# Performance work log

Hardware: AMD Instinct MI355X
Metric: run time of the kernel (lower is better)

## Reference

```python
import jax, jax.numpy as jnp
import numpy as np

B_SZ, L, D_MODEL = 2, 2048, 1024
EXPAND, N_STATE, K = 2, 16, 4
D_INNER = D_MODEL * EXPAND


def setup_inputs() -> dict:
    key = jax.random.key(0)
    ks = jax.random.split(key, 12)
    s = lambda k, shape, scale=0.02: jax.random.normal(k, shape, jnp.float32) * scale
    return {
        "x": jax.random.normal(ks[0], (B_SZ, L, D_MODEL), jnp.float32),
        "ln_gamma": jnp.ones((D_MODEL,), jnp.float32),
        "ln_beta": jnp.zeros((D_MODEL,), jnp.float32),
        "W_in": s(ks[1], (D_MODEL, 2 * D_INNER)),
        "conv_w": s(ks[2], (D_INNER, 1, K), 0.1),
        "conv_b": jnp.zeros((D_INNER,), jnp.float32),
        "A_log": jax.random.normal(ks[3], (N_STATE,), jnp.float32),
        "B_mat": s(ks[4], (N_STATE, D_INNER), 0.05),
        "C_mat": s(ks[5], (D_INNER, N_STATE), 0.05),
        "D_vec": s(ks[6], (D_INNER,), 0.1),
        "Wd": s(ks[7], (D_INNER, D_INNER)),
        "bd": jnp.zeros((D_INNER,), jnp.float32),
        "W_out": s(ks[8], (D_INNER, D_MODEL)),
    }


def _layernorm(x, g, b, eps=1e-5):
    mu = jnp.mean(x, axis=-1, keepdims=True)
    var = jnp.var(x, axis=-1, keepdims=True)
    return (x - mu) * jax.lax.rsqrt(var + eps) * g + b


def _selective_scan(x, delta, A, B_mat, C_mat, D_vec):
    # x: (b,l,d), delta: (b,l), A: (n,)
    dA = jnp.exp(delta[..., None] * A)            # (b,l,n)
    Bx = jnp.einsum('bld,nd->bln', x, B_mat) * delta[..., None]  # (b,l,n)

    def step(h, inp):
        dA_t, Bx_t = inp
        h = dA_t * h + Bx_t
        return h, h

    h0 = jnp.zeros((x.shape[0], A.shape[0]), x.dtype)
    # scan over seq axis
    _, hs = jax.lax.scan(step, h0, (jnp.swapaxes(dA, 0, 1), jnp.swapaxes(Bx, 0, 1)))
    hs = jnp.swapaxes(hs, 0, 1)                   # (b,l,n)
    return jnp.einsum('bln,dn->bld', hs, C_mat) + D_vec * x


def reference(x, ln_gamma, ln_beta, W_in, conv_w, conv_b, A_log, B_mat, C_mat, D_vec, Wd, bd, W_out):
    residual = x
    h = _layernorm(x, ln_gamma, ln_beta)
    xg = h @ W_in                                  # (b,l,2*d_inner)
    xs, gate = jnp.split(xg, 2, axis=-1)
    # depthwise causal conv (torch pads K-1 both sides then slices [:L] == left pad K-1)
    xc = jnp.swapaxes(xs, 1, 2)                    # (b,d,l)
    xc = jax.lax.conv_general_dilated(
        xc, conv_w, window_strides=(1,), padding=((K - 1, 0),),
        dimension_numbers=('NCH', 'OIH', 'NCH'), feature_group_count=D_INNER)
    xc = xc + conv_b[None, :, None]
    xs = jnp.swapaxes(xc, 1, 2)                    # (b,l,d)
    xs = jax.nn.silu(xs)
    # S4 kernel
    delta = jnp.mean(jax.nn.softplus(xs @ Wd + bd), axis=-1)  # (b,l)
    A = -jnp.exp(A_log)
    y = _selective_scan(xs, delta, A, B_mat, C_mat, D_vec)
    y = y * jax.nn.silu(gate)
    y = y @ W_out
    return residual + y
```

## Files before the change

kernel.cpp:

```cpp
#include <hip/hip_runtime.h>
#include <cstdint>
#include <cstddef>

typedef unsigned short u16;
typedef __attribute__((ext_vector_type(4))) float floatx4;
typedef __attribute__((ext_vector_type(8))) __bf16 bf16x8;

__device__ __forceinline__ float u2f(u16 u) {
    union { unsigned int i; float f; } x;
    x.i = ((unsigned int)u) << 16;
    return x.f;
}
__device__ __forceinline__ u16 f2u(float f) {
    union { float f; unsigned int i; } x;
    x.f = f;
    unsigned int r = x.i + 0x7fffu + ((x.i >> 16) & 1u);
    return (u16)(r >> 16);
}

__device__ __forceinline__ void swz(int bid, int& x, int& y) {
    int xcd = bid & 7;
    int lid = bid >> 3;
    x = lid >> 2;
    y = xcd * 4 + (lid & 3);
}

__device__ __forceinline__ void tr_tile(const float* __restrict__ in, u16* __restrict__ out,
                                        int K, int N, int bx, int by, float* tile ) {
    int n0 = bx * 32, k0 = by * 32;
    int t = threadIdx.x;
    int r = t >> 3, c4 = (t & 7) * 4;
    float4 v = *(const float4*)(in + (size_t)(k0 + r) * N + n0 + c4);
    tile[r * 33 + c4 + 0] = v.x;
    tile[r * 33 + c4 + 1] = v.y;
    tile[r * 33 + c4 + 2] = v.z;
    tile[r * 33 + c4 + 3] = v.w;
    __syncthreads();
    int n = t >> 3, kg = (t & 7) * 4;
    ushort4 o;
    o.x = f2u(tile[(kg + 0) * 33 + n]);
    o.y = f2u(tile[(kg + 1) * 33 + n]);
    o.z = f2u(tile[(kg + 2) * 33 + n]);
    o.w = f2u(tile[(kg + 3) * 33 + n]);
    *(ushort4*)(out + (size_t)(n0 + n) * K + k0 + kg) = o;
}

__global__ __launch_bounds__(256)
void prep_kernel(const float* __restrict__ W_in, u16* __restrict__ Wt_in,
                 const float* __restrict__ Wd, u16* __restrict__ Wt_ext,
                 const float* __restrict__ W_out, u16* __restrict__ Wt_out,
                 const float* __restrict__ B_mat,
                 const float* __restrict__ x, const float* __restrict__ gamma,
                 const float* __restrict__ beta, u16* __restrict__ h,
                 float* __restrict__ out) {
    __shared__ float tile[32 * 33];
    int blk = blockIdx.x, t = threadIdx.x;
    if (blk < 4096) {
        tr_tile(W_in, Wt_in, 1024, 4096, blk & 127, blk >> 7, tile);
    } else if (blk < 8192) {
        int b2 = blk - 4096;
        tr_tile(Wd, Wt_ext, 2048, 2048, b2 & 63, b2 >> 6, tile);
    } else if (blk < 10240) {
        int b3 = blk - 8192;
        tr_tile(W_out, Wt_out, 2048, 1024, b3 & 31, b3 >> 5, tile);
    } else if (blk < 14336) {
        int r = blk - 10240;
        const float4* xr = (const float4*)(x + (size_t)r * 1024);
        float4 xv = xr[t];
        ((float4*)(out + (size_t)r * 1024))[t] = xv;
        float s = xv.x + xv.y + xv.z + xv.w;
        float ss = xv.x * xv.x + xv.y * xv.y + xv.z * xv.z + xv.w * xv.w;
#pragma unroll
        for (int off = 32; off > 0; off >>= 1) {
            s += __shfl_down(s, off, 64);
            ss += __shfl_down(ss, off, 64);
        }
        __shared__ float rs[4], rss[4], mu_s, ri_s;
        int wave = t >> 6, lane = t & 63;
        if (lane == 0) { rs[wave] = s; rss[wave] = ss; }
        __syncthreads();
        if (t == 0) {
            float S = rs[0] + rs[1] + rs[2] + rs[3];
            float SS = rss[0] + rss[1] + rss[2] + rss[3];
            float mu = S * (1.f / 1024.f);
            float var = SS * (1.f / 1024.f) - mu * mu;
            mu_s = mu;
            ri_s = rsqrtf(fmaxf(var, 0.f) + 1e-5f);
        }
        __syncthreads();
        float mu = mu_s, ri = ri_s;
        float4 gv = ((const float4*)gamma)[t];
        float4 bv = ((const float4*)beta)[t];
        ushort4 o;
        o.x = f2u((xv.x - mu) * ri * gv.x + bv.x);
        o.y = f2u((xv.y - mu) * ri * gv.y + bv.y);
        o.z = f2u((xv.z - mu) * ri * gv.z + bv.z);
        o.w = f2u((xv.w - mu) * ri * gv.w + bv.w);
        ((ushort4*)(h + (size_t)r * 1024))[t] = o;
    } else {
        int idx = (blk - 14336) * 256 + t;
        int row = 2048 + (idx >> 11), col = idx & 2047;
        u16 v = (row < 2064) ? f2u(B_mat[(size_t)(row - 2048) * 2048 + col]) : (u16)0;
        Wt_ext[(size_t)row * 2048 + col] = v;
    }
}

__device__ __forceinline__ void gl_lds16(const u16* g, u16* l) {
    __builtin_amdgcn_global_load_lds(
        (const __attribute__((address_space(1))) void*)g,
        (__attribute__((address_space(3))) void*)l, 16, 0, 0);
}

template <int EPI>
__device__ __forceinline__
void gemm128_body(const u16* __restrict__ A, const u16* __restrict__ Bt,
                  void* __restrict__ out, int M, int N, int K, int Ksub) {
    __shared__ u16 As[128 * 64];
    __shared__ u16 Bs[128 * 64];
    int bx, by;
    swz(blockIdx.x, bx, by);
    const int tid = threadIdx.x;
    const int wave = tid >> 6, lane = tid & 63;
    const int row0 = by * 128, col0 = bx * 128;
    const int koff = blockIdx.y * Ksub;
    const int l16 = lane & 15, q = lane >> 4;
    const int sRow = lane >> 2, sK = (lane & 3) * 8;

    floatx4 acc[4][4];
#pragma unroll
    for (int i = 0; i < 4; ++i)
#pragma unroll
        for (int j = 0; j < 4; ++j) acc[i][j] = (floatx4){0.f, 0.f, 0.f, 0.f};

    const u16* gA = A + (size_t)(row0 + wave * 32 + sRow) * K + koff + sK;
    const u16* gB = Bt + (size_t)(col0 + wave * 32 + sRow) * K + koff + sK;
    u16* lA = As + wave * 1024;
    u16* lB = Bs + wave * 1024;
    const int rowb = (wave >> 1) * 64, colb = (wave & 1) * 64;

    for (int k0 = 0; k0 < Ksub; k0 += 64) {
#pragma unroll
        for (int h = 0; h < 2; ++h) {
            gl_lds16(gA + h * 32, lA + h * 4096);
            gl_lds16(gA + (size_t)16 * K + h * 32, lA + h * 4096 + 512);
            gl_lds16(gB + h * 32, lB + h * 4096);
            gl_lds16(gB + (size_t)16 * K + h * 32, lB + h * 4096 + 512);
        }
        gA += 64; gB += 64;
        __syncthreads();
#pragma unroll
        for (int h = 0; h < 2; ++h) {
            bf16x8 af[4], bfr[4];
#pragma unroll
            for (int mi = 0; mi < 4; ++mi)
                af[mi] = *(const bf16x8*)(As + h * 4096 + (rowb + mi * 16 + l16) * 32 + q * 8);
#pragma unroll
            for (int ni = 0; ni < 4; ++ni)
                bfr[ni] = *(const bf16x8*)(Bs + h * 4096 + (colb + ni * 16 + l16) * 32 + q * 8);
#pragma unroll
            for (int mi = 0; mi < 4; ++mi)
#pragma unroll
                for (int ni = 0; ni < 4; ++ni)
                    acc[mi][ni] = __builtin_amdgcn_mfma_f32_16x16x32_bf16(
                        af[mi], bfr[ni], acc[mi][ni], 0, 0, 0);
        }
        __syncthreads();
    }

    const int mB = row0 + rowb;
    const int nB = col0 + colb + l16;
    if constexpr (EPI == 0) {
        u16* o = (u16*)out;
#pragma unroll
        for (int mi = 0; mi < 4; ++mi)
#pragma unroll
            for (int ni = 0; ni < 4; ++ni)
#pragma unroll
                for (int rr = 0; rr < 4; ++rr)
                    o[(size_t)(mB + mi * 16 + q * 4 + rr) * N + nB + ni * 16] =
                        f2u(acc[mi][ni][rr]);
    } else if constexpr (EPI == 2) {
        float* o = (float*)out;
#pragma unroll
        for (int mi = 0; mi < 4; ++mi)
#pragma unroll
            for (int ni = 0; ni < 4; ++ni)
#pragma unroll
                for (int rr = 0; rr < 4; ++rr)
                    o[(size_t)(mB + mi * 16 + q * 4 + rr) * N + nB + ni * 16] =
                        acc[mi][ni][rr];
    } else {
        float* C = (float*)out;
#pragma unroll
        for (int mi = 0; mi < 4; ++mi)
#pragma unroll
            for (int ni = 0; ni < 4; ++ni)
#pragma unroll
                for (int rr = 0; rr < 4; ++rr)
                    atomicAdd(&C[(size_t)(mB + mi * 16 + q * 4 + rr) * N + nB + ni * 16],
                              acc[mi][ni][rr]);
    }
}

__global__ __launch_bounds__(256)
void gemm_xg(const u16* __restrict__ A, const u16* __restrict__ Bt,
             u16* __restrict__ out, int M, int N, int K) {
    gemm128_body<0>(A, Bt, out, M, N, K, K);
}

__global__ __launch_bounds__(256)
void gemm_fin(const u16* __restrict__ A, const u16* __restrict__ Bt,
              void* __restrict__ out, int M, int N, int K, int Ksub) {
    gemm128_body<4>(A, Bt, out, M, N, K, Ksub);
}

__global__ __launch_bounds__(256)
void gemm_fin_pl(const u16* __restrict__ A, const u16* __restrict__ Bt,
                 float* __restrict__ planes, int M, int N, int K, int Ksub) {
    float* plane = planes + (size_t)blockIdx.y * M * N;
    gemm128_body<2>(A, Bt, plane, M, N, K, Ksub);
}

__global__ __launch_bounds__(256)
void fin_reduce(const float* __restrict__ planes, float* __restrict__ out) {
    const size_t idx = ((size_t)blockIdx.x * 256 + threadIdx.x) * 4;
    const float4 p0 = *(const float4*)(planes + idx);
    const float4 p1 = *(const float4*)(planes + (size_t)4096 * 1024 + idx);
    float4 o = *(const float4*)(out + idx);
    o.x += p0.x + p1.x;
    o.y += p0.y + p1.y;
    o.z += p0.z + p1.z;
    o.w += p0.w + p1.w;
    *(float4*)(out + idx) = o;
}

__global__ __launch_bounds__(256)
void gemm_delta_sk(const u16* __restrict__ A, const u16* __restrict__ Bt,
                   u16* __restrict__ planes, int M, int N, int K, int Ksub) {
    u16* plane = planes + (size_t)blockIdx.y * M * N;
    gemm128_body<0>(A, Bt, plane, M, N, K, Ksub);
}

__global__ __launch_bounds__(256)
void delta_reduce(const u16* __restrict__ planes, const float* __restrict__ bias,
                  float* __restrict__ dacc, float* __restrict__ Bdotn) {
    const int r = blockIdx.x;
    const int t = threadIdx.x;
    const size_t PL = (size_t)4096 * 2176;
    const u16* p0 = planes + (size_t)r * 2176 + t * 8;
    const u16* p1 = p0 + PL;
    ushort4 a0 = *(const ushort4*)p0;
    ushort4 a1 = *(const ushort4*)(p0 + 4);
    ushort4 b0 = *(const ushort4*)p1;
    ushort4 b1 = *(const ushort4*)(p1 + 4);
    float4 c0 = *(const float4*)(bias + t * 8);
    float4 c1 = *(const float4*)(bias + t * 8 + 4);
    float e[8];
    e[0] = u2f(a0.x) + u2f(b0.x) + c0.x;
    e[1] = u2f(a0.y) + u2f(b0.y) + c0.y;
    e[2] = u2f(a0.z) + u2f(b0.z) + c0.z;
    e[3] = u2f(a0.w) + u2f(b0.w) + c0.w;
    e[4] = u2f(a1.x) + u2f(b1.x) + c1.x;
    e[5] = u2f(a1.y) + u2f(b1.y) + c1.y;
    e[6] = u2f(a1.z) + u2f(b1.z) + c1.z;
    e[7] = u2f(a1.w) + u2f(b1.w) + c1.w;
    float sv = 0.f;
#pragma unroll
    for (int i = 0; i < 8; ++i)
        sv += (e[i] > 20.f) ? e[i] : log1pf(expf(e[i]));
#pragma unroll
    for (int off = 32; off > 0; off >>= 1)
        sv += __shfl_down(sv, off, 64);
    __shared__ float wsum[4];
    const int wave = t >> 6, lane = t & 63;
    if (lane == 0) wsum[wave] = sv;
    __syncthreads();
    if (t == 0) dacc[r] = wsum[0] + wsum[1] + wsum[2] + wsum[3];
    if (t < 16) {
        const u16* q = planes + (size_t)r * 2176 + 2048 + t;
        Bdotn[(size_t)t * 4096 + r] = u2f(*q) + u2f(*(q + PL));
    }
}

__global__ __launch_bounds__(256)
void gemm_delta(const u16* __restrict__ A, const u16* __restrict__ Bt,
                float* __restrict__ dacc, const float* __restrict__ bias,
                float* __restrict__ Bdotn, int M, int N, int K) {
    __shared__ u16 As[128 * 128];
    __shared__ u16 Bs[64 * 128];
    int bx, by;
    swz(blockIdx.x, bx, by);
    const int tid = threadIdx.x;
    const int wave = tid >> 6, lane = tid & 63;
    const int row0 = by * 128, col0 = bx * 64;
    const int l16 = lane & 15, q = lane >> 4;
    const int sRow = lane >> 2, sK = (lane & 3) * 8;

    floatx4 acc[2][4];
#pragma unroll
    for (int i = 0; i < 2; ++i)
#pragma unroll
        for (int j = 0; j < 4; ++j) acc[i][j] = (floatx4){0.f, 0.f, 0.f, 0.f};

    const u16* gA = A + (size_t)(row0 + wave * 32 + sRow) * K + sK;
    const u16* gB = Bt + (size_t)(col0 + wave * 16 + sRow) * K + sK;
    u16* lA = As + wave * 1024;
    u16* lB = Bs + wave * 512;
    const int rowb = wave * 32;

    for (int k0 = 0; k0 < K; k0 += 128) {
#pragma unroll
        for (int h = 0; h < 4; ++h) {
            gl_lds16(gA + h * 32, lA + h * 4096);
            gl_lds16(gA + (size_t)16 * K + h * 32, lA + h * 4096 + 512);
            gl_lds16(gB + h * 32, lB + h * 2048);
        }
        gA += 128; gB += 128;
        __syncthreads();
#pragma unroll
        for (int h = 0; h < 4; ++h) {
            bf16x8 af[2], bfr[4];
#pragma unroll
            for (int mi = 0; mi < 2; ++mi)
                af[mi] = *(const bf16x8*)(As + h * 4096 + (rowb + mi * 16 + l16) * 32 + q * 8);
#pragma unroll
            for (int ni = 0; ni < 4; ++ni)
                bfr[ni] = *(const bf16x8*)(Bs + h * 2048 + (ni * 16 + l16) * 32 + q * 8);
#pragma unroll
            for (int mi = 0; mi < 2; ++mi)
#pragma unroll
                for (int ni = 0; ni < 4; ++ni)
                    acc[mi][ni] = __builtin_amdgcn_mfma_f32_16x16x32_bf16(
                        af[mi], bfr[ni], acc[mi][ni], 0, 0, 0);
        }
        __syncthreads();
    }

    const int mB = row0 + rowb;
    const int nB = col0 + l16;
    if (col0 < 2048) {
#pragma unroll
        for (int mi = 0; mi < 2; ++mi) {
#pragma unroll
            for (int rr = 0; rr < 4; ++rr) {
                float sv = 0.f;
#pragma unroll
                for (int ni = 0; ni < 4; ++ni) {
                    float t2 = acc[mi][ni][rr] + bias[nB + ni * 16];
                    sv += (t2 > 20.f) ? t2 : log1pf(expf(t2));
                }
#pragma unroll
                for (int off = 1; off < 16; off <<= 1)
                    sv += __shfl_xor(sv, off, 64);
                if (l16 == 0)
                    atomicAdd(&dacc[mB + mi * 16 + q * 4 + rr], sv);
            }
        }
    } else {
#pragma unroll
        for (int mi = 0; mi < 2; ++mi)
#pragma unroll
            for (int rr = 0; rr < 4; ++rr)
                Bdotn[(size_t)l16 * 4096 + mB + mi * 16 + q * 4 + rr] =
                    acc[mi][0][rr];
    }
}

__global__ __launch_bounds__(256) void conv_silu_kernel(const u16* __restrict__ xg,
                                                        const float* __restrict__ conv_w,
                                                        const float* __restrict__ conv_b,
                                                        u16* __restrict__ xsc,
                                                        float* __restrict__ delta_acc) {
    int r0 = blockIdx.x * 8;
    int l0 = r0 & 2047, bb = r0 >> 11;
    int t = threadIdx.x, d8 = t * 8;
    if (t < 8) delta_acc[r0 + t] = 0.f;

    ushort4 rw[11][2];
#pragma unroll
    for (int j = 0; j < 11; ++j) {
        int ls = l0 + j - 3;
        if (ls >= 0) {
            const u16* row = xg + (size_t)((bb << 11) + ls) * 4096 + d8;
            rw[j][0] = *(const ushort4*)row;
            rw[j][1] = *(const ushort4*)(row + 4);
        } else {
            rw[j][0] = (ushort4){0, 0, 0, 0};
            rw[j][1] = (ushort4){0, 0, 0, 0};
        }
    }
    float w[8][4];
#pragma unroll
    for (int j = 0; j < 8; ++j) {
        float4 wv = *(const float4*)(conv_w + (size_t)(d8 + j) * 4);
        w[j][0] = wv.x; w[j][1] = wv.y; w[j][2] = wv.z; w[j][3] = wv.w;
    }
    float cb[8];
    {
        float4 b0 = *(const float4*)(conv_b + d8);
        float4 b1 = *(const float4*)(conv_b + d8 + 4);
        cb[0] = b0.x; cb[1] = b0.y; cb[2] = b0.z; cb[3] = b0.w;
        cb[4] = b1.x; cb[5] = b1.y; cb[6] = b1.z; cb[7] = b1.w;
    }
#pragma unroll
    for (int i = 0; i < 8; ++i) {
        float xs[8];
#pragma unroll
        for (int j = 0; j < 8; ++j) xs[j] = cb[j];
#pragma unroll
        for (int k = 0; k < 4; ++k) {
            ushort4 u0 = rw[i + k][0], u1 = rw[i + k][1];
            xs[0] += w[0][k] * u2f(u0.x); xs[1] += w[1][k] * u2f(u0.y);
            xs[2] += w[2][k] * u2f(u0.z); xs[3] += w[3][k] * u2f(u0.w);
            xs[4] += w[4][k] * u2f(u1.x); xs[5] += w[5][k] * u2f(u1.y);
            xs[6] += w[6][k] * u2f(u1.z); xs[7] += w[7][k] * u2f(u1.w);
        }
        ushort4 o0, o1;
        o0.x = f2u(xs[0] / (1.f + expf(-xs[0])));
        o0.y = f2u(xs[1] / (1.f + expf(-xs[1])));
        o0.z = f2u(xs[2] / (1.f + expf(-xs[2])));
        o0.w = f2u(xs[3] / (1.f + expf(-xs[3])));
        o1.x = f2u(xs[4] / (1.f + expf(-xs[4])));
        o1.y = f2u(xs[5] / (1.f + expf(-xs[5])));
        o1.z = f2u(xs[6] / (1.f + expf(-xs[6])));
        o1.w = f2u(xs[7] / (1.f + expf(-xs[7])));
        u16* orow = xsc + (size_t)(r0 + i) * 2048 + d8;
        *(ushort4*)orow = o0;
        *(ushort4*)(orow + 4) = o1;
    }
}

__global__ __launch_bounds__(256) void scan_kernel(const float* __restrict__ delta_acc,
                                                   const float* __restrict__ Bdotn,
                                                   const float* __restrict__ A_log,
                                                   float* __restrict__ hsn) {
    int chain = blockIdx.x;
    int b = chain >> 4, n = chain & 15;
    int t = threadIdx.x;
    int wave = t >> 6, lane = t & 63;
    __shared__ float sd[2048], sb[2048];
    __shared__ float wA[4], wB[4];
#pragma unroll
    for (int m = 0; m < 2; ++m) {
        int idx = (m * 256 + t) * 4;
        *(float4*)(sd + idx) = *(const float4*)(delta_acc + b * 2048 + idx);
        *(float4*)(sb + idx) = *(const float4*)(Bdotn + (size_t)n * 4096 + b * 2048 + idx);
    }
    __syncthreads();
    float An = -expf(A_log[n]);
    int base = t * 8;
    float a[8], bb[8];
#pragma unroll
    for (int i = 0; i < 8; ++i) {
        float dl = sd[base + i] * (1.f / 2048.f);
        a[i] = expf(dl * An);
        bb[i] = sb[base + i] * dl;
    }
    float Aacc = 1.f, Bacc = 0.f;
#pragma unroll
    for (int i = 0; i < 8; ++i) {
        Bacc = a[i] * Bacc + bb[i];
        Aacc = a[i] * Aacc;
    }
#pragma unroll
    for (int d = 1; d < 64; d <<= 1) {
        float Ap = __shfl_up(Aacc, d, 64);
        float Bp = __shfl_up(Bacc, d, 64);
        if (lane >= d) {
            Bacc = Aacc * Bp + Bacc;
            Aacc = Aacc * Ap;
        }
    }
    if (lane == 63) { wA[wave] = Aacc; wB[wave] = Bacc; }
    float eA = __shfl_up(Aacc, 1, 64);
    float eB = __shfl_up(Bacc, 1, 64);
    if (lane == 0) { eA = 1.f; eB = 0.f; }
    __syncthreads();
    float pB = 0.f;
#pragma unroll
    for (int w = 0; w < 3; ++w)
        if (w < wave) pB = wA[w] * pB + wB[w];
    float h = eA * pB + eB;
#pragma unroll
    for (int i = 0; i < 8; ++i) {
        h = a[i] * h + bb[i];
        sd[base + i] = h;
    }
    __syncthreads();
#pragma unroll
    for (int m = 0; m < 2; ++m) {
        int idx = (m * 256 + t) * 4;
        *(float4*)(hsn + (size_t)n * 4096 + b * 2048 + idx) = *(const float4*)(sd + idx);
    }
}

__global__ __launch_bounds__(256) void ymid_kernel(const float* __restrict__ hsn,
                                                   const float* __restrict__ C_mat,
                                                   const float* __restrict__ D_vec,
                                                   const u16* __restrict__ xsc,
                                                   const u16* __restrict__ xg,
                                                   u16* __restrict__ ymid) {
    const int t = threadIdx.x;
    const int d0 = blockIdx.x * 512 + t * 2;
    const int r0 = blockIdx.y * 32;
    __shared__ float hsv[32 * 16];
#pragma unroll
    for (int k = 0; k < 2; ++k) {
        int idx = t * 2 + k;
        int rl = idx >> 4, nn = idx & 15;
        hsv[idx] = hsn[(size_t)nn * 4096 + r0 + rl];
    }
    float c0[16], c1[16];
#pragma unroll
    for (int k = 0; k < 4; ++k) {
        float4 v0 = *(const float4*)(C_mat + (size_t)d0 * 16 + k * 4);
        float4 v1 = *(const float4*)(C_mat + (size_t)(d0 + 1) * 16 + k * 4);
        c0[k * 4 + 0] = v0.x; c0[k * 4 + 1] = v0.y; c0[k * 4 + 2] = v0.z; c0[k * 4 + 3] = v0.w;
        c1[k * 4 + 0] = v1.x; c1[k * 4 + 1] = v1.y; c1[k * 4 + 2] = v1.z; c1[k * 4 + 3] = v1.w;
    }
    const float dv0 = D_vec[d0], dv1 = D_vec[d0 + 1];
    __syncthreads();
#pragma unroll 4
    for (int rl = 0; rl < 32; ++rl) {
        const int r = r0 + rl;
        float h0 = 0.f, h1 = 0.f;
#pragma unroll
        for (int nn = 0; nn < 16; ++nn) {
            float hv = hsv[rl * 16 + nn];
            h0 += hv * c0[nn];
            h1 += hv * c1[nn];
        }
        unsigned int xv = *(const unsigned int*)(xsc + (size_t)r * 2048 + d0);
        unsigned int gv = *(const unsigned int*)(xg + (size_t)r * 4096 + 2048 + d0);
        float x0 = u2f((u16)(xv & 0xffffu)), x1 = u2f((u16)(xv >> 16));
        float g0 = u2f((u16)(gv & 0xffffu)), g1 = u2f((u16)(gv >> 16));
        float y0 = (h0 + dv0 * x0) * (g0 / (1.f + expf(-g0)));
        float y1 = (h1 + dv1 * x1) * (g1 / (1.f + expf(-g1)));
        unsigned int o = (unsigned int)f2u(y0) | ((unsigned int)f2u(y1) << 16);
        *(unsigned int*)(ymid + (size_t)r * 2048 + d0) = o;
    }
}

extern "C" void kernel_launch(void* const* d_in, const int* in_sizes, int n_in,
                              void* d_out, int out_size, void* d_ws, size_t ws_size,
                              hipStream_t stream) {
    (void)in_sizes; (void)n_in;
    const float* x      = (const float*)d_in[0];
    const float* ln_g   = (const float*)d_in[1];
    const float* ln_b   = (const float*)d_in[2];
    const float* W_in   = (const float*)d_in[3];
    const float* conv_w = (const float*)d_in[4];
    const float* conv_b = (const float*)d_in[5];
    const float* A_log  = (const float*)d_in[6];
    const float* B_mat  = (const float*)d_in[7];
    const float* C_mat  = (const float*)d_in[8];
    const float* D_vec  = (const float*)d_in[9];
    const float* Wd     = (const float*)d_in[10];
    const float* bd     = (const float*)d_in[11];
    const float* W_out  = (const float*)d_in[12];
    float* out = (float*)d_out;

    char* base = (char*)d_ws;
    u16* Wt_in  = (u16*)base;
    u16* h_ln   = (u16*)base + 4096ull * 1024;
    u16* ymid   = (u16*)base;
    u16* Wt_ext = (u16*)(base + (16ull << 20));
    u16* Wt_out = (u16*)(base + (25ull << 20));
    u16* xg     = (u16*)(base + (29ull << 20));
    u16* xsc    = (u16*)(base + (61ull << 20));
    float* delta_acc = (float*)(base + (77ull << 20));
    float* Bdotn = delta_acc + 4096;
    float* hsn   = Bdotn + 16 * 4096;
    u16* planes  = (u16*)(base + (78ull << 20));
    float* fplanes = (float*)(base + (78ull << 20));
    size_t needed = (77ull << 20) + 4096ull * 4 * (1 + 2 * 16);
    size_t needed_sk = (78ull << 20) + 2ull * 4096 * 2176 * 2;

    if (needed > ws_size) {
        hipMemsetAsync(d_out, 0x7F, (size_t)out_size * 4, stream);
        return;
    }
    const bool use_sk = (ws_size >= needed_sk);

    prep_kernel<<<14848, 256, 0, stream>>>(W_in, Wt_in, Wd, Wt_ext, W_out, Wt_out,
                                           B_mat, x, ln_g, ln_b, h_ln, out);
    gemm_xg<<<1024, 256, 0, stream>>>(h_ln, Wt_in, xg, 4096, 4096, 1024);
    conv_silu_kernel<<<512, 256, 0, stream>>>(xg, conv_w, conv_b, xsc, delta_acc);
    if (use_sk) {
        gemm_delta_sk<<<dim3(544, 2), 256, 0, stream>>>(xsc, Wt_ext, planes,
                                                        4096, 2176, 2048, 1024);
        delta_reduce<<<4096, 256, 0, stream>>>(planes, bd, delta_acc, Bdotn);
    } else {
        gemm_delta<<<1056, 256, 0, stream>>>(xsc, Wt_ext, delta_acc, bd, Bdotn,
                                             4096, 2112, 2048);
    }
    scan_kernel<<<32, 256, 0, stream>>>(delta_acc, Bdotn, A_log, hsn);
    ymid_kernel<<<dim3(4, 128), 256, 0, stream>>>(hsn, C_mat, D_vec, xsc, xg, ymid);
    if (use_sk) {
        gemm_fin_pl<<<dim3(256, 2), 256, 0, stream>>>(ymid, Wt_out, fplanes,
                                                      4096, 1024, 2048, 1024);
        fin_reduce<<<4096, 256, 0, stream>>>(fplanes, out);
    } else {
        gemm_fin<<<dim3(256, 2), 256, 0, stream>>>(ymid, Wt_out, out, 4096, 1024, 2048, 1024);
    }
}
```

Before: 324.4 us.

## Use 4-way bf16 split-K planes for output GEMM and halve conv/ymid tiles

Increases split-K for the final GEMM from 2 to 4 planes and stores the partial planes as bf16 instead of fp32. The reduce kernel now sums four bf16 planes eight elements per thread. The conv and ymid kernels each process half as many rows per block and launch twice as many blocks, to raise occupancy and parallelism. Storing partials in bf16 adds rounding error to the output projection.

```diff
diff --git a/kernel.cpp b/kernel.cpp
--- a/kernel.cpp
+++ b/kernel.cpp
@@ -179,16 +179,6 @@
                 for (int rr = 0; rr < 4; ++rr)
                     o[(size_t)(mB + mi * 16 + q * 4 + rr) * N + nB + ni * 16] =
                         f2u(acc[mi][ni][rr]);
-    } else if constexpr (EPI == 2) {
-        float* o = (float*)out;
-#pragma unroll
-        for (int mi = 0; mi < 4; ++mi)
-#pragma unroll
-            for (int ni = 0; ni < 4; ++ni)
-#pragma unroll
-                for (int rr = 0; rr < 4; ++rr)
-                    o[(size_t)(mB + mi * 16 + q * 4 + rr) * N + nB + ni * 16] =
-                        acc[mi][ni][rr];
     } else {
         float* C = (float*)out;
 #pragma unroll
@@ -216,22 +206,29 @@
 
 __global__ __launch_bounds__(256)
 void gemm_fin_pl(const u16* __restrict__ A, const u16* __restrict__ Bt,
-                 float* __restrict__ planes, int M, int N, int K, int Ksub) {
-    float* plane = planes + (size_t)blockIdx.y * M * N;
-    gemm128_body<2>(A, Bt, plane, M, N, K, Ksub);
-}
-
-__global__ __launch_bounds__(256)
-void fin_reduce(const float* __restrict__ planes, float* __restrict__ out) {
-    const size_t idx = ((size_t)blockIdx.x * 256 + threadIdx.x) * 4;
-    const float4 p0 = *(const float4*)(planes + idx);
-    const float4 p1 = *(const float4*)(planes + (size_t)4096 * 1024 + idx);
-    float4 o = *(const float4*)(out + idx);
-    o.x += p0.x + p1.x;
-    o.y += p0.y + p1.y;
-    o.z += p0.z + p1.z;
-    o.w += p0.w + p1.w;
-    *(float4*)(out + idx) = o;
+                 u16* __restrict__ planes, int M, int N, int K, int Ksub) {
+    u16* plane = planes + (size_t)blockIdx.y * M * N;
+    gemm128_body<0>(A, Bt, plane, M, N, K, Ksub);
+}
+
+__global__ __launch_bounds__(256)
+void fin_reduce(const u16* __restrict__ planes, float* __restrict__ out) {
+    const size_t PL = (size_t)4096 * 1024;
+    const size_t idx = ((size_t)blockIdx.x * 256 + threadIdx.x) * 8;
+    float acc[8] = {0.f, 0.f, 0.f, 0.f, 0.f, 0.f, 0.f, 0.f};
+#pragma unroll
+    for (int p = 0; p < 4; ++p) {
+        ushort4 v0 = *(const ushort4*)(planes + p * PL + idx);
+        ushort4 v1 = *(const ushort4*)(planes + p * PL + idx + 4);
+        acc[0] += u2f(v0.x); acc[1] += u2f(v0.y); acc[2] += u2f(v0.z); acc[3] += u2f(v0.w);
+        acc[4] += u2f(v1.x); acc[5] += u2f(v1.y); acc[6] += u2f(v1.z); acc[7] += u2f(v1.w);
+    }
+    float4 o0 = *(const float4*)(out + idx);
+    float4 o1 = *(const float4*)(out + idx + 4);
+    o0.x += acc[0]; o0.y += acc[1]; o0.z += acc[2]; o0.w += acc[3];
+    o1.x += acc[4]; o1.y += acc[5]; o1.z += acc[6]; o1.w += acc[7];
+    *(float4*)(out + idx) = o0;
+    *(float4*)(out + idx + 4) = o1;
 }
 
 __global__ __launch_bounds__(256)
@@ -371,14 +368,14 @@
                                                         const float* __restrict__ conv_b,
                                                         u16* __restrict__ xsc,
                                                         float* __restrict__ delta_acc) {
-    int r0 = blockIdx.x * 8;
+    int r0 = blockIdx.x * 4;
     int l0 = r0 & 2047, bb = r0 >> 11;
     int t = threadIdx.x, d8 = t * 8;
-    if (t < 8) delta_acc[r0 + t] = 0.f;
-
-    ushort4 rw[11][2];
-#pragma unroll
-    for (int j = 0; j < 11; ++j) {
+    if (t < 4) delta_acc[r0 + t] = 0.f;
+
+    ushort4 rw[7][2];
+#pragma unroll
+    for (int j = 0; j < 7; ++j) {
         int ls = l0 + j - 3;
         if (ls >= 0) {
             const u16* row = xg + (size_t)((bb << 11) + ls) * 4096 + d8;
@@ -403,7 +400,7 @@
         cb[4] = b1.x; cb[5] = b1.y; cb[6] = b1.z; cb[7] = b1.w;
     }
 #pragma unroll
-    for (int i = 0; i < 8; ++i) {
+    for (int i = 0; i < 4; ++i) {
         float xs[8];
 #pragma unroll
         for (int j = 0; j < 8; ++j) xs[j] = cb[j];
@@ -502,13 +499,11 @@
                                                    u16* __restrict__ ymid) {
     const int t = threadIdx.x;
     const int d0 = blockIdx.x * 512 + t * 2;
-    const int r0 = blockIdx.y * 32;
-    __shared__ float hsv[32 * 16];
-#pragma unroll
-    for (int k = 0; k < 2; ++k) {
-        int idx = t * 2 + k;
-        int rl = idx >> 4, nn = idx & 15;
-        hsv[idx] = hsn[(size_t)nn * 4096 + r0 + rl];
+    const int r0 = blockIdx.y * 16;
+    __shared__ float hsv[16 * 16];
+    {
+        int rl = t >> 4, nn = t & 15;
+        hsv[t] = hsn[(size_t)nn * 4096 + r0 + rl];
     }
     float c0[16], c1[16];
 #pragma unroll
@@ -521,7 +516,7 @@
     const float dv0 = D_vec[d0], dv1 = D_vec[d0 + 1];
     __syncthreads();
 #pragma unroll 4
-    for (int rl = 0; rl < 32; ++rl) {
+    for (int rl = 0; rl < 16; ++rl) {
         const int r = r0 + rl;
         float h0 = 0.f, h1 = 0.f;
 #pragma unroll
@@ -572,7 +567,7 @@
     float* Bdotn = delta_acc + 4096;
     float* hsn   = Bdotn + 16 * 4096;
     u16* planes  = (u16*)(base + (78ull << 20));
-    float* fplanes = (float*)(base + (78ull << 20));
+    u16* fplanes = (u16*)(base + (78ull << 20));
     size_t needed = (77ull << 20) + 4096ull * 4 * (1 + 2 * 16);
     size_t needed_sk = (78ull << 20) + 2ull * 4096 * 2176 * 2;
 
@@ -585,7 +580,7 @@
     prep_kernel<<<14848, 256, 0, stream>>>(W_in, Wt_in, Wd, Wt_ext, W_out, Wt_out,
                                            B_mat, x, ln_g, ln_b, h_ln, out);
     gemm_xg<<<1024, 256, 0, stream>>>(h_ln, Wt_in, xg, 4096, 4096, 1024);
-    conv_silu_kernel<<<512, 256, 0, stream>>>(xg, conv_w, conv_b, xsc, delta_acc);
+    conv_silu_kernel<<<1024, 256, 0, stream>>>(xg, conv_w, conv_b, xsc, delta_acc);
     if (use_sk) {
         gemm_delta_sk<<<dim3(544, 2), 256, 0, stream>>>(xsc, Wt_ext, planes,
                                                         4096, 2176, 2048, 1024);
@@ -595,11 +590,11 @@
                                              4096, 2112, 2048);
     }
     scan_kernel<<<32, 256, 0, stream>>>(delta_acc, Bdotn, A_log, hsn);
-    ymid_kernel<<<dim3(4, 128), 256, 0, stream>>>(hsn, C_mat, D_vec, xsc, xg, ymid);
+    ymid_kernel<<<dim3(4, 256), 256, 0, stream>>>(hsn, C_mat, D_vec, xsc, xg, ymid);
     if (use_sk) {
-        gemm_fin_pl<<<dim3(256, 2), 256, 0, stream>>>(ymid, Wt_out, fplanes,
-                                                      4096, 1024, 2048, 1024);
-        fin_reduce<<<4096, 256, 0, stream>>>(fplanes, out);
+        gemm_fin_pl<<<dim3(256, 4), 256, 0, stream>>>(ymid, Wt_out, fplanes,
+                                                      4096, 1024, 2048, 512);
+        fin_reduce<<<2048, 256, 0, stream>>>(fplanes, out);
     } else {
         gemm_fin<<<dim3(256, 2), 256, 0, stream>>>(ymid, Wt_out, out, 4096, 1024, 2048, 1024);
     }
```

Measured after the change: 325.5 us. Within noise of the previous version (+0.3%).
